# Optimization experiments

Hardware: AMD Instinct MI355X
Metric: run time of the kernel (lower is better)

## Reference

```python
import jax, jax.numpy as jnp
import numpy as np
import math

LN_EPS = 1e-5
EPS = 1e-8

def _unfold3(x, stride):
    # torch nn.Unfold(kernel_size=3, stride=stride, padding=1); output [B, C*9, L]
    B, C, H, W = x.shape
    xp = jnp.pad(x, ((0, 0), (0, 0), (1, 1), (1, 1)))
    Ho = (H + 2 - 3) // stride + 1
    Wo = (W + 2 - 3) // stride + 1
    pats = [xp[:, :, i:i + stride * (Ho - 1) + 1:stride, j:j + stride * (Wo - 1) + 1:stride]
            for i in range(3) for j in range(3)]
    out = jnp.stack(pats, axis=2)  # [B,C,9,Ho,Wo]  (c-major, then kh,kw: torch ordering)
    return out.reshape(B, C * 9, Ho * Wo)

def _ln(x, g, b):
    mu = jnp.mean(x, axis=-1, keepdims=True)
    var = jnp.mean((x - mu) ** 2, axis=-1, keepdims=True)
    return (x - mu) * jax.lax.rsqrt(var + LN_EPS) * g + b

def _prm_exp(x, w):
    # x: [B,T,emb], w: [m,emb] -> [B,T,m]
    m = w.shape[0]
    xd = jnp.sum(x * x, axis=-1, keepdims=True) / 2.0
    wtx = jnp.einsum('bte,me->btm', x, w)
    return jnp.exp(wtx - xd) / math.sqrt(m)

def _performer(x, kqv_w, kqv_b, pw, pb, g1, b1, g2, b2, m1w, m1b, m2w, m2b, w):
    # Token_performer.forward (dropout = identity, eval mode)
    h = _ln(x, g1, b1)
    kqv = h @ kqv_w.T + kqv_b
    k, q, v = jnp.split(kqv, 3, axis=-1)  # torch.split order: k, q, v
    kp = _prm_exp(k, w)
    qp = _prm_exp(q, w)
    D = jnp.einsum('btm,bm->bt', qp, kp.sum(axis=1))[..., None]        # [B,T,1]
    kptv = jnp.einsum('btn,btm->bnm', v, kp)                            # [B,emb,m]
    y = jnp.einsum('btm,bnm->btn', qp, kptv) / (D + EPS)                # [B,T,emb]
    y = v + (y @ pw.T + pb)
    h2 = _ln(y, g2, b2)
    mlp = jax.nn.gelu(h2 @ m1w.T + m1b, approximate=False) @ m2w.T + m2b
    return y + mlp

def _forward(x,
             p1_kqv_w, p1_kqv_b, p1_proj_w, p1_proj_b, p1_n1_g, p1_n1_b, p1_n2_g, p1_n2_b,
             p1_m1_w, p1_m1_b, p1_m2_w, p1_m2_b, p1_w,
             p2_kqv_w, p2_kqv_b, p2_proj_w, p2_proj_b, p2_n1_g, p2_n1_b, p2_n2_g, p2_n2_b,
             p2_m1_w, p2_m1_b, p2_m2_w, p2_m2_b, p2_w,
             proj_w, proj_b):
    t = _unfold3(x, 1).transpose(0, 2, 1)  # [B, 50176, 27]
    t = _performer(t, p1_kqv_w, p1_kqv_b, p1_proj_w, p1_proj_b, p1_n1_g, p1_n1_b,
                   p1_n2_g, p1_n2_b, p1_m1_w, p1_m1_b, p1_m2_w, p1_m2_b, p1_w)
    B, N, C = t.shape
    s = int(math.isqrt(N))
    t = t.transpose(0, 2, 1).reshape(B, C, s, s)
    t = _unfold3(t, 2).transpose(0, 2, 1)  # [B, 12544, 576]
    t = _performer(t, p2_kqv_w, p2_kqv_b, p2_proj_w, p2_proj_b, p2_n1_g, p2_n1_b,
                   p2_n2_g, p2_n2_b, p2_m1_w, p2_m1_b, p2_m2_w, p2_m2_b, p2_w)
    B, N, C = t.shape
    s = int(math.isqrt(N))
    t = t.transpose(0, 2, 1).reshape(B, C, s, s)
    t = _unfold3(t, 2).transpose(0, 2, 1)  # [B, 3136, 576]
    return t @ proj_w.T + proj_b           # [B, 3136, 768]

def setup_inputs() -> dict:
    key = jax.random.key(0)
    ks = iter(jax.random.split(key, 40))
    def rn(shape, scale=0.02):
        return (jax.random.normal(next(ks), shape, dtype=jnp.float32) * scale)
    EMB, M = 64, 32
    inp = {'x': jax.random.normal(next(ks), (8, 3, 224, 224), dtype=jnp.float32)}
    for pfx, dim in (('p1', 27), ('p2', 576)):
        inp[f'{pfx}_kqv_w'] = rn((3 * EMB, dim))
        inp[f'{pfx}_kqv_b'] = jnp.zeros((3 * EMB,), jnp.float32)
        inp[f'{pfx}_proj_w'] = rn((EMB, EMB))
        inp[f'{pfx}_proj_b'] = jnp.zeros((EMB,), jnp.float32)
        inp[f'{pfx}_n1_g'] = jnp.ones((dim,), jnp.float32)
        inp[f'{pfx}_n1_b'] = jnp.zeros((dim,), jnp.float32)
        inp[f'{pfx}_n2_g'] = jnp.ones((EMB,), jnp.float32)
        inp[f'{pfx}_n2_b'] = jnp.zeros((EMB,), jnp.float32)
        inp[f'{pfx}_m1_w'] = rn((EMB, EMB))
        inp[f'{pfx}_m1_b'] = jnp.zeros((EMB,), jnp.float32)
        inp[f'{pfx}_m2_w'] = rn((EMB, EMB))
        inp[f'{pfx}_m2_b'] = jnp.zeros((EMB,), jnp.float32)
        # frozen random-feature projection, scaled ~ orthogonal * sqrt(m)
        inp[f'{pfx}_w'] = jax.random.normal(next(ks), (M, EMB), dtype=jnp.float32)
    inp['proj_w'] = rn((768, 576))
    inp['proj_b'] = jnp.zeros((768,), jnp.float32)
    return inp

def reference(x,
              p1_kqv_w, p1_kqv_b, p1_proj_w, p1_proj_b, p1_n1_g, p1_n1_b, p1_n2_g, p1_n2_b,
              p1_m1_w, p1_m1_b, p1_m2_w, p1_m2_b, p1_w,
              p2_kqv_w, p2_kqv_b, p2_proj_w, p2_proj_b, p2_n1_g, p2_n1_b, p2_n2_g, p2_n2_b,
              p2_m1_w, p2_m1_b, p2_m2_w, p2_m2_b, p2_w,
              proj_w, proj_b):
    return _forward(x,
                    p1_kqv_w, p1_kqv_b, p1_proj_w, p1_proj_b, p1_n1_g, p1_n1_b, p1_n2_g, p1_n2_b,
                    p1_m1_w, p1_m1_b, p1_m2_w, p1_m2_b, p1_w,
                    p2_kqv_w, p2_kqv_b, p2_proj_w, p2_proj_b, p2_n1_g, p2_n1_b, p2_n2_g, p2_n2_b,
                    p2_m1_w, p2_m1_b, p2_m2_w, p2_m2_b, p2_w,
                    proj_w, proj_b)
```

## Files before the change

### kernel.cpp

```cpp
#include <hip/hip_runtime.h>
#include <hip/hip_bf16.h>
#include <math.h>

typedef __hip_bfloat16 bf16;
typedef __attribute__((ext_vector_type(8))) short frag8;
typedef __attribute__((ext_vector_type(4))) float f32x4;
typedef long long ll;

__device__ __forceinline__ float b2f(bf16 v) { return __bfloat162float(v); }
__device__ __forceinline__ bf16 f2b(float v) { return __float2bfloat16(v); }

__device__ __forceinline__ unsigned pk2f(float a, float b) {
    union { bf16 h[2]; unsigned u; } c;
    c.h[0] = f2b(a); c.h[1] = f2b(b);
    return c.u;
}
__device__ __forceinline__ void up8(const bf16* p, float* f) {
    const uint4 u = *(const uint4*)p;
    union { unsigned u; bf16 h[2]; } c;
    c.u = u.x; f[0] = b2f(c.h[0]); f[1] = b2f(c.h[1]);
    c.u = u.y; f[2] = b2f(c.h[0]); f[3] = b2f(c.h[1]);
    c.u = u.z; f[4] = b2f(c.h[0]); f[5] = b2f(c.h[1]);
    c.u = u.w; f[6] = b2f(c.h[0]); f[7] = b2f(c.h[1]);
}
__device__ __forceinline__ void up8u(const uint4 u, float* f) {
    union { unsigned u; bf16 h[2]; } c;
    c.u = u.x; f[0] = b2f(c.h[0]); f[1] = b2f(c.h[1]);
    c.u = u.y; f[2] = b2f(c.h[0]); f[3] = b2f(c.h[1]);
    c.u = u.z; f[4] = b2f(c.h[0]); f[5] = b2f(c.h[1]);
    c.u = u.w; f[6] = b2f(c.h[0]); f[7] = b2f(c.h[1]);
}

#define LN_EPS 1e-5f
#define D_EPS 1e-8f
#define INV_SQRT_M 0.17677669529663687f

__global__ __launch_bounds__(256) void k_sniff(const void* x, int* mode)
{
    __shared__ int cnt;
    if (threadIdx.x == 0) cnt = 0;
    __syncthreads();
    const unsigned short* u = (const unsigned short*)x;
    const unsigned short h = u[2 * threadIdx.x];
    const unsigned int bits = ((unsigned int)h) << 16;
    const float v = __uint_as_float(bits);
    const float a = fabsf(v);
    const bool sane = (h == 0) || (a >= 1e-8f && a <= 1e4f);
    if (!sane) atomicAdd(&cnt, 1);
    __syncthreads();
    if (threadIdx.x == 0) *mode = (cnt > 64) ? 1 : 0;
}

struct CvTab { const void* src[28]; int dstOff[28]; int cum[29]; };

__global__ __launch_bounds__(256) void k_convert_all(CvTab tab, bf16* base,
                                                     const int* mode)
{
    const int idx = blockIdx.x * 256 + threadIdx.x;
    if (idx >= tab.cum[28]) return;
    int s = 0;
    while (idx >= tab.cum[s + 1]) ++s;
    const int local = idx - tab.cum[s];
    const float v = (*mode) ? ((const float*)tab.src[s])[local]
                            : b2f(((const bf16*)tab.src[s])[local]);
    base[tab.dstOff[s] + local] = f2b(v);
}

__global__ __launch_bounds__(256) void k_prep(
    const void* __restrict__ w1raw, const int* __restrict__ mode,
    bf16* __restrict__ w1ph, bf16* __restrict__ w1pl)
{
    const int idx = blockIdx.x * 256 + threadIdx.x;
    if (idx >= 6144) return;
    const int o = idx >> 5, k = idx & 31;
    float v = 0.f;
    if (k < 27)
        v = (*mode) ? ((const float*)w1raw)[o * 27 + k]
                    : b2f(((const bf16*)w1raw)[o * 27 + k]);
    const bf16 h = f2b(v);
    w1ph[idx] = h;
    w1pl[idx] = f2b(v - b2f(h));
}

__global__ __launch_bounds__(256) void k_fused1(
    const bf16* __restrict__ x, const bf16* __restrict__ w1ph,
    const bf16* __restrict__ w1pl, const bf16* __restrict__ kqvb,
    const bf16* __restrict__ n1g, const bf16* __restrict__ n1b,
    const bf16* __restrict__ pw,
    bf16* __restrict__ KP, bf16* __restrict__ QP, bf16* __restrict__ V,
    float* __restrict__ red, const int b)
{
    __shared__ __align__(16) char smem[49632];
    bf16 (*wps)[72] = (bf16(*)[72])(smem);
    bf16 (*Ah)[40]  = (bf16(*)[40])(smem + 4608);
    bf16 (*Al)[40]  = (bf16(*)[40])(smem + 9728);
    bf16 (*Th)[72]  = (bf16(*)[72])(smem + 14848);
    bf16 (*Tl)[72]  = (bf16(*)[72])(smem + 24064);
    bf16 (*Wh)[40]  = (bf16(*)[40])(smem + 33280);
    bf16 (*Wl)[40]  = (bf16(*)[40])(smem + 38400);
    bf16 (*KPs)[40] = (bf16(*)[40])(smem + 43520);
    bf16 (*Vs)[72]  = (bf16(*)[72])(smem + 14848);
    float* kbs = (float*)(smem + 48640);
    float* gs  = (float*)(smem + 49408);
    float* bs  = (float*)(smem + 49520);

    const int tid = threadIdx.x;
    {
        const int i = tid * 8;
        *(uint4*)(&wps[i >> 6][i & 63]) = *(const uint4*)(pw + i);
    }
    if (tid < 192) kbs[tid] = b2f(kqvb[tid]);
    if (tid < 27) { gs[tid] = b2f(n1g[tid]); bs[tid] = b2f(n1b[tid]); }
    if (blockIdx.x == 0)
        for (int i = tid; i < 2080; i += 256) red[i] = 0.f;

    const int tok = tid >> 2, part = tid & 3;
    const int t = blockIdx.x * 64 + tok;
    const int h = t / 224, w = t - h * 224;
    const int d0 = part * 7;
    const int nd = (part == 3) ? 6 : 7;
    float vals[7];
    float s = 0.f;
    #pragma unroll
    for (int q = 0; q < 7; ++q) {
        float val = 0.f;
        if (q < nd) {
            const int d = d0 + q;
            const int c = d / 9, rr = d - c * 9;
            const int pi = rr / 3, pj = rr - pi * 3;
            const int hh = h + pi - 1, ww = w + pj - 1;
            if (hh >= 0 && hh < 224 && ww >= 0 && ww < 224)
                val = b2f(x[((ll)(b * 3 + c) * 224 + hh) * 224 + ww]);
        }
        vals[q] = val; s += val;
    }
    s += __shfl_xor(s, 1, 64);  s += __shfl_xor(s, 2, 64);
    const float mean = s * (1.f / 27.f);
    float s2 = 0.f;
    #pragma unroll
    for (int q = 0; q < 7; ++q) {
        if (q < nd) { const float dd = vals[q] - mean; s2 += dd * dd; }
    }
    s2 += __shfl_xor(s2, 1, 64); s2 += __shfl_xor(s2, 2, 64);
    const float rs = rsqrtf(s2 * (1.f / 27.f) + LN_EPS);
    __syncthreads();
    #pragma unroll
    for (int q = 0; q < 7; ++q) {
        if (q < nd) {
            const int d = d0 + q;
            const float nv = (vals[q] - mean) * rs * gs[d] + bs[d];
            const bf16 nh = f2b(nv);
            Ah[tok][d] = nh;
            Al[tok][d] = f2b(nv - b2f(nh));
        }
    }
    if (part == 3) {
        #pragma unroll
        for (int d = 27; d < 32; ++d) { Ah[tok][d] = f2b(0.f); Al[tok][d] = f2b(0.f); }
    }

    const int wv = tid >> 6, lane = tid & 63;
    const int l15 = lane & 15;
    const int k8 = (lane >> 4) << 3;
    const int rbase = (lane >> 4) << 2;
    const int srow = tid >> 2;
    const int scol = (tid & 3) << 3;
    const int colg = (tid & 3) << 4;

    float xdK[4], xdQ[4];

    #pragma unroll
    for (int g = 0; g < 3; ++g) {
        *(uint4*)(&Wh[srow][scol]) = *(const uint4*)(w1ph + (g * 64 + srow) * 32 + scol);
        *(uint4*)(&Wl[srow][scol]) = *(const uint4*)(w1pl + (g * 64 + srow) * 32 + scol);
        __syncthreads();
        const frag8 ah = *(const frag8*)(&Ah[(wv << 4) + l15][k8]);
        const frag8 al = *(const frag8*)(&Al[(wv << 4) + l15][k8]);
        f32x4 acc[4] = {};
        #pragma unroll
        for (int nt = 0; nt < 4; ++nt) {
            const frag8 bh = *(const frag8*)(&Wh[(nt << 4) + l15][k8]);
            const frag8 bl = *(const frag8*)(&Wl[(nt << 4) + l15][k8]);
            acc[nt] = __builtin_amdgcn_mfma_f32_16x16x32_bf16(ah, bh, acc[nt], 0, 0, 0);
            acc[nt] = __builtin_amdgcn_mfma_f32_16x16x32_bf16(al, bh, acc[nt], 0, 0, 0);
            acc[nt] = __builtin_amdgcn_mfma_f32_16x16x32_bf16(ah, bl, acc[nt], 0, 0, 0);
            acc[nt] = __builtin_amdgcn_mfma_f32_16x16x32_bf16(al, bl, acc[nt], 0, 0, 0);
        }
        float xdp[4] = {0.f, 0.f, 0.f, 0.f};
        #pragma unroll
        for (int nt = 0; nt < 4; ++nt) {
            const int col = (nt << 4) + l15;
            const float bv = kbs[g * 64 + col];
            #pragma unroll
            for (int r = 0; r < 4; ++r) {
                const float tb = acc[nt][r] + bv;
                const int trow = (wv << 4) + rbase + r;
                if (g < 2) {
                    const bf16 th = f2b(tb);
                    Th[trow][col] = th;
                    Tl[trow][col] = f2b(tb - b2f(th));
                    xdp[r] += tb * tb;
                } else {
                    Vs[trow][col] = f2b(tb);
                }
            }
        }
        if (g < 2) {
            #pragma unroll
            for (int r = 0; r < 4; ++r) {
                float v = xdp[r];
                v += __shfl_xor(v, 1, 64); v += __shfl_xor(v, 2, 64);
                v += __shfl_xor(v, 4, 64); v += __shfl_xor(v, 8, 64);
                if (g == 0) xdK[r] = 0.5f * v; else xdQ[r] = 0.5f * v;
            }
        }
        __syncthreads();
        if (g < 2) {
            f32x4 acc2[2] = {};
            #pragma unroll
            for (int k0 = 0; k0 < 64; k0 += 32) {
                const frag8 ath = *(const frag8*)(&Th[(wv << 4) + l15][k8 + k0]);
                const frag8 atl = *(const frag8*)(&Tl[(wv << 4) + l15][k8 + k0]);
                #pragma unroll
                for (int nt = 0; nt < 2; ++nt) {
                    const frag8 bw = *(const frag8*)(&wps[(nt << 4) + l15][k8 + k0]);
                    acc2[nt] = __builtin_amdgcn_mfma_f32_16x16x32_bf16(ath, bw, acc2[nt], 0, 0, 0);
                    acc2[nt] = __builtin_amdgcn_mfma_f32_16x16x32_bf16(atl, bw, acc2[nt], 0, 0, 0);
                }
            }
            #pragma unroll
            for (int nt = 0; nt < 2; ++nt)
                #pragma unroll
                for (int r = 0; r < 4; ++r) {
                    const float xd = (g == 0) ? xdK[r] : xdQ[r];
                    const float p = expf(fminf(acc2[nt][r] - xd, 30.f)) * INV_SQRT_M;
                    KPs[(wv << 4) + rbase + r][(nt << 4) + l15] = f2b(p);
                }
            __syncthreads();
            bf16* dstP = (g == 0 ? KP : QP) + ((ll)blockIdx.x * 64 + srow) * 32 + scol;
            *(uint4*)dstP = *(const uint4*)(&KPs[srow][scol]);
            __syncthreads();
        } else {
            bf16* dstV = V + ((ll)blockIdx.x * 64 + srow) * 64 + colg;
            *(uint4*)dstV       = *(const uint4*)(&Vs[srow][colg]);
            *(uint4*)(dstV + 8) = *(const uint4*)(&Vs[srow][colg + 8]);
        }
    }
}

__global__ __launch_bounds__(256) void k_reduce(
    const bf16* __restrict__ kpB, const bf16* __restrict__ vB, const int vstride,
    const int T, float* __restrict__ redBase, const int chunk)
{
    __shared__ bf16 VT[64][72];
    __shared__ bf16 KT[32][72];
    const int bz = blockIdx.y;
    const bf16* kp = kpB + (ll)bz * T * 32;
    const bf16* v  = vB + (ll)bz * T * (ll)vstride;
    float* red = redBase + (ll)bz * 2080;
    const int tid = threadIdx.x;
    const int wv = tid >> 6, lane = tid & 63;
    const int l15 = lane & 15, k8 = (lane >> 4) << 3, rbase = (lane >> 4) << 2;
    const int t0 = blockIdx.x * chunk;

    frag8 ones;
    {
        union { bf16 h; short s; } u; u.h = f2b(1.f);
        #pragma unroll
        for (int i = 0; i < 8; ++i) ones[i] = u.s;
    }

    f32x4 acc[2] = {};
    f32x4 accK[2] = {};

    for (int tt = 0; tt < chunk; tt += 64) {
        const int tb = t0 + tt;
        __syncthreads();
        {
            const int tk = tid >> 2, n0 = (tid & 3) << 4;
            const bf16* src = v + (ll)(tb + tk) * vstride + n0;
            bf16 tmp[16];
            *(uint4*)tmp       = *(const uint4*)src;
            *(uint4*)(tmp + 8) = *(const uint4*)(src + 8);
            #pragma unroll
            for (int j = 0; j < 16; ++j) VT[n0 + j][tk] = tmp[j];
        }
        {
            const int tk = tid >> 2, m0 = (tid & 3) << 3;
            const bf16* src = kp + (ll)(tb + tk) * 32 + m0;
            bf16 tmp[8];
            *(uint4*)tmp = *(const uint4*)src;
            #pragma unroll
            for (int j = 0; j < 8; ++j) KT[m0 + j][tk] = tmp[j];
        }
        __syncthreads();
        #pragma unroll
        for (int ks = 0; ks < 2; ++ks) {
            const frag8 af = *(const frag8*)(&VT[(wv << 4) + l15][k8 + ks * 32]);
            #pragma unroll
            for (int tn = 0; tn < 2; ++tn) {
                const frag8 bfv = *(const frag8*)(&KT[(tn << 4) + l15][k8 + ks * 32]);
                acc[tn] = __builtin_amdgcn_mfma_f32_16x16x32_bf16(af, bfv, acc[tn], 0, 0, 0);
            }
            if (wv == 0) {
                #pragma unroll
                for (int tn = 0; tn < 2; ++tn) {
                    const frag8 bfv = *(const frag8*)(&KT[(tn << 4) + l15][k8 + ks * 32]);
                    accK[tn] = __builtin_amdgcn_mfma_f32_16x16x32_bf16(ones, bfv, accK[tn], 0, 0, 0);
                }
            }
        }
    }
    #pragma unroll
    for (int tn = 0; tn < 2; ++tn) {
        const int m = (tn << 4) + l15;
        #pragma unroll
        for (int r = 0; r < 4; ++r) {
            const int n = (wv << 4) + rbase + r;
            atomicAdd(&red[n * 32 + m], acc[tn][r]);
        }
    }
    if (wv == 0 && (lane >> 4) == 0) {
        #pragma unroll
        for (int tn = 0; tn < 2; ++tn)
            atomicAdd(&red[2048 + (tn << 4) + l15], accK[tn][0]);
    }
}

__global__ __launch_bounds__(256) void k_postmlp(
    const bf16* __restrict__ qpB, const float* __restrict__ redBase,
    const bf16* __restrict__ vB, const int vstride,
    const bf16* __restrict__ pw, const bf16* __restrict__ pb,
    const bf16* __restrict__ n2g, const bf16* __restrict__ n2b,
    const bf16* __restrict__ w1, const bf16* __restrict__ b1,
    const bf16* __restrict__ w2, const bf16* __restrict__ b2,
    bf16* outB, const int T)
{
    __shared__ __align__(16) char smem[47232];
    bf16 (*QPs)[40] = (bf16(*)[40])(smem);
    bf16 (*KH)[40]  = (bf16(*)[40])(smem + 5120);
    bf16 (*KL)[40]  = (bf16(*)[40])(smem + 10240);
    float (*Cs)[72] = (float(*)[72])(smem);
    bf16 (*W1s)[72] = (bf16(*)[72])(smem);
    bf16 (*W2s)[72] = (bf16(*)[72])(smem + 9216);
    bf16 (*PWs)[72] = (bf16(*)[72])(smem + 18432);
    bf16 (*Gs)[72]  = (bf16(*)[72])(smem + 18432);
    bf16 (*Y0H)[72] = (bf16(*)[72])(smem + 27648);
    bf16 (*Ys)[72]  = (bf16(*)[72])(smem + 27648);
    bf16 (*Y0L)[72] = (bf16(*)[72])(smem + 36864);
    bf16 (*Hn)[72]  = (bf16(*)[72])(smem + 36864);
    float* invs  = (float*)(smem + 46080);
    float* pbs   = (float*)(smem + 46336);
    float* ksums = (float*)(smem + 46592);
    float* mns   = (float*)(smem + 46720);
    float* rss   = (float*)(smem + 46976);

    const int tid = threadIdx.x;
    const int bz = blockIdx.y;
    const float* red = redBase + (ll)bz * 2080;
    const bf16* qp = qpB + (ll)bz * (ll)T * 32;
    const bf16* v  = vB + (ll)bz * (ll)T * (ll)vstride;
    bf16* out = outB + (ll)bz * (ll)T * 64;
    const ll m0 = (ll)blockIdx.x * 64;

    const int lr = tid >> 2;
    const int lc8 = (tid & 3) << 3;
    const int lc16 = (tid & 3) << 4;

    *(uint4*)(&QPs[lr][lc8]) = *(const uint4*)(qp + (m0 + lr) * 32 + lc8);
    *(uint4*)(&PWs[lr][lc16])     = *(const uint4*)(pw + lr * 64 + lc16);
    *(uint4*)(&PWs[lr][lc16 + 8]) = *(const uint4*)(pw + lr * 64 + lc16 + 8);
    {
        const int i0 = tid * 8;
        const float4 a = *(const float4*)(red + i0);
        const float4 b = *(const float4*)(red + i0 + 4);
        const int n = i0 >> 5, m = i0 & 31;
        float xs[8] = {a.x, a.y, a.z, a.w, b.x, b.y, b.z, b.w};
        #pragma unroll
        for (int k = 0; k < 8; ++k) {
            const bf16 h = f2b(xs[k]);
            KH[n][m + k] = h;
            KL[n][m + k] = f2b(xs[k] - b2f(h));
        }
    }
    if (tid < 32) ksums[tid] = red[2048 + tid];
    if (tid < 64) pbs[tid] = b2f(pb[tid]);
    __syncthreads();

    if (tid < 64) {
        float D = D_EPS;
        #pragma unroll
        for (int m = 0; m < 32; ++m) D += b2f(QPs[tid][m]) * ksums[m];
        invs[tid] = 1.f / D;
    }

    const int wv = tid >> 6, lane = tid & 63;
    const int l15 = lane & 15;
    const int mr = (wv << 4) + l15;
    const int k8 = (lane >> 4) << 3;
    const int rbase = (lane >> 4) << 2;

    f32x4 acc[4] = {};
    {
        const frag8 af = *(const frag8*)(&QPs[mr][k8]);
        #pragma unroll
        for (int tn = 0; tn < 4; ++tn) {
            const int nr = (tn << 4) + l15;
            const frag8 bh = *(const frag8*)(&KH[nr][k8]);
            acc[tn] = __builtin_amdgcn_mfma_f32_16x16x32_bf16(af, bh, acc[tn], 0, 0, 0);
            const frag8 bl = *(const frag8*)(&KL[nr][k8]);
            acc[tn] = __builtin_amdgcn_mfma_f32_16x16x32_bf16(af, bl, acc[tn], 0, 0, 0);
        }
    }
    #pragma unroll
    for (int tn = 0; tn < 4; ++tn) {
        const int n = (tn << 4) + l15;
        #pragma unroll
        for (int r = 0; r < 4; ++r) {
            const float x = acc[tn][r];
            const bf16 h = f2b(x);
            Y0H[(wv << 4) + rbase + r][n] = h;
            Y0L[(wv << 4) + rbase + r][n] = f2b(x - b2f(h));
        }
    }
    __syncthreads();

    f32x4 acc2[4] = {};
    #pragma unroll
    for (int k0 = 0; k0 < 64; k0 += 32) {
        const frag8 ah = *(const frag8*)(&Y0H[mr][k8 + k0]);
        const frag8 al = *(const frag8*)(&Y0L[mr][k8 + k0]);
        #pragma unroll
        for (int tn = 0; tn < 4; ++tn) {
            const frag8 bw = *(const frag8*)(&PWs[(tn << 4) + l15][k8 + k0]);
            acc2[tn] = __builtin_amdgcn_mfma_f32_16x16x32_bf16(ah, bw, acc2[tn], 0, 0, 0);
            acc2[tn] = __builtin_amdgcn_mfma_f32_16x16x32_bf16(al, bw, acc2[tn], 0, 0, 0);
        }
    }
    #pragma unroll
    for (int tn = 0; tn < 4; ++tn) {
        const int n = (tn << 4) + l15;
        #pragma unroll
        for (int r = 0; r < 4; ++r) {
            const int row = (wv << 4) + rbase + r;
            Cs[row][n] = acc2[tn][r] * invs[row] + pbs[n];
        }
    }
    __syncthreads();

    {
        const int row = tid >> 2;
        const bf16* vsrc = v + (m0 + row) * (ll)vstride + lc16;
        #pragma unroll
        for (int hh = 0; hh < 2; ++hh) {
            float vv[8];
            up8(vsrc + hh * 8, vv);
            const float* cp = &Cs[row][lc16 + hh * 8];
            uint4 st;
            st.x = pk2f(cp[0] + vv[0], cp[1] + vv[1]);
            st.y = pk2f(cp[2] + vv[2], cp[3] + vv[3]);
            st.z = pk2f(cp[4] + vv[4], cp[5] + vv[5]);
            st.w = pk2f(cp[6] + vv[6], cp[7] + vv[7]);
            *(uint4*)(&Ys[row][lc16 + hh * 8]) = st;
        }
    }
    __syncthreads();

    if (tid < 64) {
        float s = 0.f, s2 = 0.f;
        #pragma unroll
        for (int n = 0; n < 64; ++n) { const float vv = b2f(Ys[tid][n]); s += vv; s2 += vv * vv; }
        const float mn = s * (1.f / 64.f);
        const float var = fmaxf(s2 * (1.f / 64.f) - mn * mn, 0.f);
        mns[tid] = mn; rss[tid] = rsqrtf(var + LN_EPS);
    }
    *(uint4*)(&W1s[lr][lc16])     = *(const uint4*)(w1 + lr * 64 + lc16);
    *(uint4*)(&W1s[lr][lc16 + 8]) = *(const uint4*)(w1 + lr * 64 + lc16 + 8);
    *(uint4*)(&W2s[lr][lc16])     = *(const uint4*)(w2 + lr * 64 + lc16);
    *(uint4*)(&W2s[lr][lc16 + 8]) = *(const uint4*)(w2 + lr * 64 + lc16 + 8);
    __syncthreads();

    for (int i = tid; i < 4096; i += 256) {
        const int r = i >> 6, c = i & 63;
        Hn[r][c] = f2b((b2f(Ys[r][c]) - mns[r]) * rss[r] * b2f(n2g[c]) + b2f(n2b[c]));
    }
    __syncthreads();

    f32x4 accm[4] = {};
    #pragma unroll
    for (int k0 = 0; k0 < 64; k0 += 32) {
        const frag8 af = *(const frag8*)(&Hn[mr][k8 + k0]);
        #pragma unroll
        for (int tn = 0; tn < 4; ++tn) {
            const frag8 bfv = *(const frag8*)(&W1s[(tn << 4) + l15][k8 + k0]);
            accm[tn] = __builtin_amdgcn_mfma_f32_16x16x32_bf16(af, bfv, accm[tn], 0, 0, 0);
        }
    }
    #pragma unroll
    for (int tn = 0; tn < 4; ++tn) {
        const int n = (tn << 4) + l15;
        const float bv = b2f(b1[n]);
        #pragma unroll
        for (int r = 0; r < 4; ++r) {
            float vg = accm[tn][r] + bv;
            vg = 0.5f * vg * (1.f + erff(vg * 0.70710678118654752f));
            Gs[(wv << 4) + rbase + r][n] = f2b(vg);
        }
    }
    __syncthreads();

    f32x4 accn[4] = {};
    #pragma unroll
    for (int k0 = 0; k0 < 64; k0 += 32) {
        const frag8 af = *(const frag8*)(&Gs[mr][k8 + k0]);
        #pragma unroll
        for (int tn = 0; tn < 4; ++tn) {
            const frag8 bfv = *(const frag8*)(&W2s[(tn << 4) + l15][k8 + k0]);
            accn[tn] = __builtin_amdgcn_mfma_f32_16x16x32_bf16(af, bfv, accn[tn], 0, 0, 0);
        }
    }
    #pragma unroll
    for (int tn = 0; tn < 4; ++tn) {
        const int n = (tn << 4) + l15;
        const float bv = b2f(b2[n]);
        #pragma unroll
        for (int r = 0; r < 4; ++r)
            Hn[(wv << 4) + rbase + r][n] = f2b(accn[tn][r] + bv);
    }
    __syncthreads();

    {
        const int row = tid >> 2;
        bf16* dst = out + (m0 + row) * 64 + lc16;
        #pragma unroll
        for (int hh = 0; hh < 2; ++hh) {
            float sv[8], rv[8];
            up8(&Hn[row][lc16 + hh * 8], sv);
            up8(&Ys[row][lc16 + hh * 8], rv);
            uint4 st;
            st.x = pk2f(sv[0] + rv[0], sv[1] + rv[1]);
            st.y = pk2f(sv[2] + rv[2], sv[3] + rv[3]);
            st.z = pk2f(sv[4] + rv[4], sv[5] + rv[5]);
            st.w = pk2f(sv[6] + rv[6], sv[7] + rv[7]);
            *(uint4*)(dst + hh * 8) = st;
        }
    }
}

__global__ __launch_bounds__(256) void k_unfold576(
    const bf16* __restrict__ in, const int Hin, const int Ho,
    const bf16* __restrict__ g, const bf16* __restrict__ bb,
    const int do_ln, bf16* __restrict__ A,
    const ll inBStride, const ll outBStride)
{
    in += (ll)blockIdx.y * inBStride;
    A  += (ll)blockIdx.y * outBStride;
    const int t = blockIdx.x * 4 + (threadIdx.x >> 6);
    const int l = threadIdx.x & 63;
    const int ho = t / Ho, wo = t - ho * Ho;
    float vals[9];
    float s = 0.f;
    #pragma unroll
    for (int r = 0; r < 9; ++r) {
        const int d = l + (r << 6);
        const int c = d / 9;
        const int rr = d - c * 9;
        const int i = rr / 3, j = rr - i * 3;
        const int hh = 2 * ho + i - 1, ww = 2 * wo + j - 1;
        float val = 0.f;
        if (hh >= 0 && hh < Hin && ww >= 0 && ww < Hin)
            val = b2f(in[((ll)hh * Hin + ww) * 64 + c]);
        vals[r] = val; s += val;
    }
    bf16* out = A + (ll)t * 576;
    if (do_ln) {
        #pragma unroll
        for (int o = 32; o > 0; o >>= 1) s += __shfl_xor(s, o, 64);
        const float mean = s * (1.f / 576.f);
        float s2 = 0.f;
        #pragma unroll
        for (int r = 0; r < 9; ++r) { const float dd = vals[r] - mean; s2 += dd * dd; }
        #pragma unroll
        for (int o = 32; o > 0; o >>= 1) s2 += __shfl_xor(s2, o, 64);
        const float rs = rsqrtf(s2 * (1.f / 576.f) + LN_EPS);
        #pragma unroll
        for (int r = 0; r < 9; ++r) {
            const int d = l + (r << 6);
            out[d] = f2b((vals[r] - mean) * rs * b2f(g[d]) + b2f(bb[d]));
        }
    } else {
        #pragma unroll
        for (int r = 0; r < 9; ++r) out[l + (r << 6)] = f2b(vals[r]);
    }
}

__global__ __launch_bounds__(256) void k_gemm(
    const bf16* __restrict__ A, const int lda,
    const bf16* __restrict__ W,
    const bf16* __restrict__ bias,
    const bf16* res, const int ldres,
    void* C, const int ldc, const ll mOff,
    const int K, const int* outm)
{
    __shared__ bf16 As[2][64][40];
    __shared__ bf16 Bs[2][64][40];
    __shared__ bf16 Cs[64][72];
    const int tid = threadIdx.x;
    const int wv = tid >> 6;
    const int lane = tid & 63;
    const ll m0 = (ll)blockIdx.x * 64;
    const int n0 = blockIdx.y * 64;
    f32x4 acc[4] = {};
    const int lr = tid >> 2;
    const int lc = (tid & 3) << 3;
    const int mr = (wv << 4) + (lane & 15);
    const int k8 = (lane >> 4) << 3;
    const bf16* Ag = A + (m0 + lr) * (ll)lda + lc;
    const bf16* Wg = W + (ll)(n0 + lr) * K + lc;

    uint4 av  = *(const uint4*)(Ag);
    uint4 wv4 = *(const uint4*)(Wg);
    *(uint4*)(&As[0][lr][lc]) = av;
    *(uint4*)(&Bs[0][lr][lc]) = wv4;
    int cur = 0;
    __syncthreads();
    for (int k0 = 0; k0 < K; k0 += 32) {
        const bool nxt = (k0 + 32 < K);
        if (nxt) {
            av  = *(const uint4*)(Ag + k0 + 32);
            wv4 = *(const uint4*)(Wg + k0 + 32);
        }
        const frag8 af = *(const frag8*)(&As[cur][mr][k8]);
        #pragma unroll
        for (int tn = 0; tn < 4; ++tn) {
            const frag8 bfv = *(const frag8*)(&Bs[cur][(tn << 4) + (lane & 15)][k8]);
            acc[tn] = __builtin_amdgcn_mfma_f32_16x16x32_bf16(af, bfv, acc[tn], 0, 0, 0);
        }
        if (nxt) {
            *(uint4*)(&As[cur ^ 1][lr][lc]) = av;
            *(uint4*)(&Bs[cur ^ 1][lr][lc]) = wv4;
        }
        __syncthreads();
        cur ^= 1;
    }
    const int om = outm ? *outm : 0;
    const int rbase = (lane >> 4) << 2;
    if (om) {
        #pragma unroll
        for (int tn = 0; tn < 4; ++tn) {
            const int n = n0 + (tn << 4) + (lane & 15);
            const float bv = bias ? b2f(bias[n]) : 0.f;
            #pragma unroll
            for (int r = 0; r < 4; ++r) {
                const ll m = m0 + (wv << 4) + rbase + r;
                float v = acc[tn][r] + bv;
                if (res) v += b2f(res[m * (ll)ldres + n]);
                ((float*)C)[(m + mOff) * (ll)ldc + n] = v;
            }
        }
        return;
    }
    #pragma unroll
    for (int tn = 0; tn < 4; ++tn) {
        const int nl = (tn << 4) + (lane & 15);
        const float bv = bias ? b2f(bias[n0 + nl]) : 0.f;
        #pragma unroll
        for (int r = 0; r < 4; ++r) {
            const ll m = m0 + (wv << 4) + rbase + r;
            float v = acc[tn][r] + bv;
            if (res) v += b2f(res[m * (ll)ldres + n0 + nl]);
            Cs[(wv << 4) + rbase + r][nl] = f2b(v);
        }
    }
    __syncthreads();
    const int row = tid >> 2;
    const int colg = (tid & 3) << 4;
    bf16* dst = (bf16*)C + (m0 + mOff + row) * (ll)ldc + n0 + colg;
    *(uint4*)dst       = *(const uint4*)(&Cs[row][colg]);
    *(uint4*)(dst + 8) = *(const uint4*)(&Cs[row][colg + 8]);
}

__global__ __launch_bounds__(256) void k_gemm128(
    const bf16* __restrict__ A, const int lda,
    const bf16* __restrict__ W,
    const bf16* __restrict__ bias,
    void* C, const int ldc, const ll mOff,
    const int K, const int* outm, const int gridN)
{
    __shared__ __align__(16) char smem[40960];
    bf16 (*As)[128][40] = (bf16(*)[128][40])smem;
    bf16 (*Bs)[128][40] = (bf16(*)[128][40])(smem + 20480);
    bf16 (*Cs)[136]     = (bf16(*)[136])smem;

    const int nwg = gridDim.x;
    const int orig = blockIdx.x;
    const int xcd = orig & 7;
    const int q = nwg >> 3, r = nwg & 7;
    const int wgid = (xcd < r ? xcd * (q + 1) : r * (q + 1) + (xcd - r) * q)
                     + (orig >> 3);
    const int mTile = wgid / gridN;
    const int nTile = wgid - mTile * gridN;
    const ll m0 = (ll)mTile * 128;
    const int n0 = nTile * 128;

    const int tid = threadIdx.x;
    const int wv = tid >> 6, lane = tid & 63, l15 = lane & 15;
    const int k8 = (lane >> 4) << 3;
    const int rbase = (lane >> 4) << 2;
    const int mr0 = (wv << 5) + l15;
    const int sr = tid >> 1, sc = (tid & 1) << 4;
    const bf16* Ag = A + (m0 + sr) * (ll)lda + sc;
    const bf16* Wg = W + (ll)(n0 + sr) * K + sc;

    f32x4 acc[2][8] = {};
    uint4 a0 = *(const uint4*)(Ag);
    uint4 a1 = *(const uint4*)(Ag + 8);
    uint4 b0 = *(const uint4*)(Wg);
    uint4 b1 = *(const uint4*)(Wg + 8);
    *(uint4*)(&(*As)[sr][sc])     = a0;
    *(uint4*)(&(*As)[sr][sc + 8]) = a1;
    *(uint4*)(&(*Bs)[sr][sc])     = b0;
    *(uint4*)(&(*Bs)[sr][sc + 8]) = b1;
    int cur = 0;
    __syncthreads();
    for (int k0 = 0; k0 < K; k0 += 32) {
        const bool nxt = (k0 + 32 < K);
        if (nxt) {
            a0 = *(const uint4*)(Ag + k0 + 32);
            a1 = *(const uint4*)(Ag + k0 + 40);
            b0 = *(const uint4*)(Wg + k0 + 32);
            b1 = *(const uint4*)(Wg + k0 + 40);
        }
        const frag8 af0 = *(const frag8*)(&As[cur][mr0][k8]);
        const frag8 af1 = *(const frag8*)(&As[cur][mr0 + 16][k8]);
        #pragma unroll
        for (int tn = 0; tn < 8; ++tn) {
            const frag8 bfv = *(const frag8*)(&Bs[cur][(tn << 4) + l15][k8]);
            acc[0][tn] = __builtin_amdgcn_mfma_f32_16x16x32_bf16(af0, bfv, acc[0][tn], 0, 0, 0);
            acc[1][tn] = __builtin_amdgcn_mfma_f32_16x16x32_bf16(af1, bfv, acc[1][tn], 0, 0, 0);
        }
        if (nxt) {
            *(uint4*)(&As[cur ^ 1][sr][sc])     = a0;
            *(uint4*)(&As[cur ^ 1][sr][sc + 8]) = a1;
            *(uint4*)(&Bs[cur ^ 1][sr][sc])     = b0;
            *(uint4*)(&Bs[cur ^ 1][sr][sc + 8]) = b1;
        }
        __syncthreads();
        cur ^= 1;
    }
    const int om = outm ? *outm : 0;
    if (om) {
        #pragma unroll
        for (int mi = 0; mi < 2; ++mi)
            #pragma unroll
            for (int tn = 0; tn < 8; ++tn) {
                const int n = n0 + (tn << 4) + l15;
                const float bv = bias ? b2f(bias[n]) : 0.f;
                #pragma unroll
                for (int rr2 = 0; rr2 < 4; ++rr2) {
                    const ll m = m0 + (wv << 5) + (mi << 4) + rbase + rr2;
                    ((float*)C)[(m + mOff) * (ll)ldc + n] = acc[mi][tn][rr2] + bv;
                }
            }
        return;
    }
    #pragma unroll
    for (int mi = 0; mi < 2; ++mi)
        #pragma unroll
        for (int tn = 0; tn < 8; ++tn) {
            const int nl = (tn << 4) + l15;
            const float bv = bias ? b2f(bias[n0 + nl]) : 0.f;
            #pragma unroll
            for (int rr2 = 0; rr2 < 4; ++rr2)
                Cs[(wv << 5) + (mi << 4) + rbase + rr2][nl] = f2b(acc[mi][tn][rr2] + bv);
        }
    __syncthreads();
    const int row = tid >> 1;
    const int colg = (tid & 1) << 6;
    bf16* dst = (bf16*)C + (m0 + mOff + row) * (ll)ldc + n0 + colg;
    #pragma unroll
    for (int u = 0; u < 8; ++u)
        *(uint4*)(dst + u * 8) = *(const uint4*)(&Cs[row][colg + u * 8]);
}

__global__ __launch_bounds__(256) void k_fusedP2(
    const bf16* __restrict__ kqv, const bf16* __restrict__ pw,
    bf16* __restrict__ KP, bf16* __restrict__ QP,
    float* __restrict__ redBase, const int T)
{
    __shared__ __align__(16) char smem[19200];
    bf16 (*Ks)[72]  = (bf16(*)[72])(smem);
    bf16 (*wps)[72] = (bf16(*)[72])(smem + 9216);
    bf16 (*KPs)[40] = (bf16(*)[40])(smem + 13824);
    float* xds = (float*)(smem + 18944);

    const int tid = threadIdx.x;
    const int bz = blockIdx.y;
    {
        const int i = tid * 8;
        *(uint4*)(&wps[i >> 6][i & 63]) = *(const uint4*)(pw + i);
    }
    if (blockIdx.x == 0) {
        float* red = redBase + (ll)bz * 2080;
        for (int i = tid; i < 2080; i += 256) red[i] = 0.f;
    }
    const ll gt0 = (ll)bz * T + (ll)blockIdx.x * 64;
    const int srow = tid >> 2;
    const int colg = (tid & 3) << 4;
    const int scol = (tid & 3) << 3;
    const int wv = tid >> 6, lane = tid & 63;
    const int l15 = lane & 15, k8 = (lane >> 4) << 3, rbase = (lane >> 4) << 2;

    #pragma unroll
    for (int p = 0; p < 2; ++p) {
        const bf16* src = kqv + (gt0 + srow) * 192 + p * 64 + colg;
        const uint4 u0 = *(const uint4*)src;
        const uint4 u1 = *(const uint4*)(src + 8);
        *(uint4*)(&Ks[srow][colg])     = u0;
        *(uint4*)(&Ks[srow][colg + 8]) = u1;
        float f0[8], f1[8];
        up8u(u0, f0); up8u(u1, f1);
        float s2 = 0.f;
        #pragma unroll
        for (int k = 0; k < 8; ++k) s2 += f0[k] * f0[k] + f1[k] * f1[k];
        s2 += __shfl_xor(s2, 1, 64); s2 += __shfl_xor(s2, 2, 64);
        if ((tid & 3) == 0) xds[srow] = 0.5f * s2;
        __syncthreads();
        f32x4 acc2[2] = {};
        #pragma unroll
        for (int k0 = 0; k0 < 64; k0 += 32) {
            const frag8 af = *(const frag8*)(&Ks[(wv << 4) + l15][k8 + k0]);
            #pragma unroll
            for (int nt = 0; nt < 2; ++nt) {
                const frag8 bw = *(const frag8*)(&wps[(nt << 4) + l15][k8 + k0]);
                acc2[nt] = __builtin_amdgcn_mfma_f32_16x16x32_bf16(af, bw, acc2[nt], 0, 0, 0);
            }
        }
        #pragma unroll
        for (int nt = 0; nt < 2; ++nt)
            #pragma unroll
            for (int r = 0; r < 4; ++r) {
                const int trow = (wv << 4) + rbase + r;
                const float pv = expf(fminf(acc2[nt][r] - xds[trow], 30.f)) * INV_SQRT_M;
                KPs[trow][(nt << 4) + l15] = f2b(pv);
            }
        __syncthreads();
        bf16* dst = (p == 0 ? KP : QP) + (gt0 + srow) * 32 + scol;
        *(uint4*)dst = *(const uint4*)(&KPs[srow][scol]);
        __syncthreads();
    }
}

extern "C" void kernel_launch(void* const* d_in, const int* in_sizes, int n_in,
                              void* d_out, int out_size, void* d_ws, size_t ws_size,
                              hipStream_t stream)
{
    (void)in_sizes; (void)n_in; (void)out_size;
    const int T1 = 50176, T2 = 12544;
    char* ws = (char*)d_ws;

    size_t cur = 0;
    auto alloc = [&](size_t bytes) {
        size_t r = cur; cur += (bytes + 127) & ~(size_t)127; return r;
    };
    static const int segIdx[28] = {0, 2, 3, 4, 5, 6, 7, 8, 9, 10, 11, 12, 13,
                                   14, 15, 16, 17, 18, 19, 20, 21, 22, 23, 24, 25, 26, 27, 28};
    static const int segN[28] = {1204224, 192, 4096, 64, 27, 27, 64, 64, 4096, 64, 4096, 64, 2048,
                                 110592, 192, 4096, 64, 576, 576, 64, 64, 4096, 64, 4096, 64, 2048,
                                 442368, 768};
    size_t segOff[28];
    for (int i = 0; i < 28; ++i) segOff[i] = alloc((size_t)segN[i] * 2);
    const size_t oMODE = alloc(256);
    const size_t oRED  = alloc(66560);
    const size_t oW1P  = alloc(24576);
    const size_t oBIG  = alloc(6422528);
    const size_t oKP   = alloc(3211264);
    const size_t oQP   = alloc(3211264);
    (void)oQP;

    bf16* P[28];
    for (int i = 0; i < 28; ++i) P[i] = (bf16*)(ws + segOff[i]);
    bf16* XC = P[0];
    bf16 *P1KQVB = P[1], *P1PW = P[2], *P1PB = P[3], *P1N1G = P[4], *P1N1B = P[5];
    bf16 *P1N2G = P[6], *P1N2B = P[7], *P1M1W = P[8], *P1M1B = P[9], *P1M2W = P[10];
    bf16 *P1M2B = P[11], *P1W = P[12];
    bf16 *P2KQVW = P[13], *P2KQVB = P[14], *P2PW = P[15], *P2PB = P[16];
    bf16 *P2N1G = P[17], *P2N1B = P[18], *P2N2G = P[19], *P2N2B = P[20];
    bf16 *P2M1W = P[21], *P2M1B = P[22], *P2M2W = P[23], *P2M2B = P[24], *P2W = P[25];
    bf16 *PROJW = P[26], *PROJB = P[27];

    int*   MODE = (int*)(ws + oMODE);
    float* REDF = (float*)(ws + oRED);
    bf16*  W1PH = (bf16*)(ws + oW1P);
    bf16*  W1PL = (bf16*)(ws + oW1P + 12288);
    bf16*  BIG  = (bf16*)(ws + oBIG);
    bf16*  KP   = (bf16*)(ws + oKP);
    bf16*  QP   = (bf16*)(ws + oKP + 3211264);
    bf16*  A2   = (bf16*)(ws + oKP);
    bf16*  KQV2F = (bf16*)d_out;
    bf16*  KP2F  = (bf16*)(ws + oKP);
    bf16*  QP2F  = (bf16*)(ws + oKP + 6422528);
    bf16*  YB2F  = (bf16*)(ws + oBIG);
    bf16*  A3c   = (bf16*)(ws + oBIG + 12845056);

    k_sniff<<<1, 256, 0, stream>>>(d_in[0], MODE);
    CvTab tab;
    int cum = 0;
    for (int i = 0; i < 28; ++i) {
        tab.src[i] = d_in[segIdx[i]];
        tab.dstOff[i] = (int)(segOff[i] / 2);
        tab.cum[i] = cum;
        cum += segN[i];
    }
    tab.cum[28] = cum;
    k_convert_all<<<(cum + 255) / 256, 256, 0, stream>>>(tab, (bf16*)ws, MODE);
    k_prep<<<24, 256, 0, stream>>>(d_in[1], MODE, W1PH, W1PL);

    for (int b = 0; b < 8; ++b) {
        float* REDb = REDF + (ll)b * 2080;
        k_fused1<<<784, 256, 0, stream>>>(XC, W1PH, W1PL, P1KQVB, P1N1G, P1N1B,
                                          P1W, KP, QP, BIG, REDb, b);
        k_reduce<<<dim3(392, 1), 256, 0, stream>>>(KP, BIG, 64, T1, REDb, 128);
        k_postmlp<<<dim3(784, 1), 256, 0, stream>>>(QP, REDb, BIG, 64, P1PW, P1PB,
            P1N2G, P1N2B, P1M1W, P1M1B, P1M2W, P1M2B, BIG, T1);
        k_unfold576<<<dim3(3136, 1), 256, 0, stream>>>(BIG, 224, 112, P2N1G, P2N1B,
                                                       1, A2, 0, 0);
        k_gemm<<<dim3(196, 3), 256, 0, stream>>>(A2, 576, P2KQVW, P2KQVB,
            nullptr, 0, KQV2F, 192, (ll)b * T2, 576, nullptr);
    }

    k_fusedP2<<<dim3(196, 8), 256, 0, stream>>>(KQV2F, P2W, KP2F, QP2F, REDF, T2);
    k_reduce<<<dim3(98, 8), 256, 0, stream>>>(KP2F, KQV2F + 128, 192, T2, REDF, 128);
    k_postmlp<<<dim3(196, 8), 256, 0, stream>>>(QP2F, REDF, KQV2F + 128, 192,
        P2PW, P2PB, P2N2G, P2N2B, P2M1W, P2M1B, P2M2W, P2M2B, YB2F, T2);

    const size_t needFull = oBIG + 12845056 + (size_t)25088 * 576 * 2;
    if (ws_size >= needFull) {
        bf16* A3 = (bf16*)(ws + oBIG + 12845056);
        k_unfold576<<<dim3(784, 8), 256, 0, stream>>>(
            YB2F, 112, 56, nullptr, nullptr, 0, A3, (ll)T2 * 64, (ll)3136 * 576);
        k_gemm128<<<1176, 256, 0, stream>>>(A3, 576, PROJW, PROJB,
            d_out, 768, 0, 576, MODE, 6);
    } else {
        for (int c = 0; c < 4; ++c) {
            k_unfold576<<<dim3(784, 2), 256, 0, stream>>>(
                YB2F + (ll)(2 * c) * T2 * 64, 112, 56, nullptr, nullptr, 0,
                A3c, (ll)T2 * 64, (ll)3136 * 576);
            k_gemm128<<<294, 256, 0, stream>>>(A3c, 576, PROJW, PROJB,
                d_out, 768, (ll)c * 6272, 576, MODE, 6);
        }
    }
}
```

Measured before the change: 963.6 us.

## Fuse stage-1 kptv/ksum reduction into k_fused1 with per-block atomics

The stage-1 reduction (V^T·KP and the KP column sum) now runs inside k_fused1 on each 64-token tile, using shared-memory transposes and MFMA, with results accumulated into the global buffer by atomics. This drops the separate k_reduce launch per batch and the write and re-read of KP through global memory. Zeroing of the reduction buffer moves to k_prep for all batches at once. In exchange there are many float atomics per block and an extra shared-memory transpose phase.

```diff
diff --git a/kernel.cpp b/kernel.cpp
--- a/kernel.cpp
+++ b/kernel.cpp
@@ -68,9 +68,10 @@
 
 __global__ __launch_bounds__(256) void k_prep(
     const void* __restrict__ w1raw, const int* __restrict__ mode,
-    bf16* __restrict__ w1ph, bf16* __restrict__ w1pl)
+    bf16* __restrict__ w1ph, bf16* __restrict__ w1pl, float* __restrict__ redf)
 {
     const int idx = blockIdx.x * 256 + threadIdx.x;
+    if (idx < 16640) redf[idx] = 0.f;
     if (idx >= 6144) return;
     const int o = idx >> 5, k = idx & 31;
     float v = 0.f;
@@ -87,7 +88,7 @@
     const bf16* __restrict__ w1pl, const bf16* __restrict__ kqvb,
     const bf16* __restrict__ n1g, const bf16* __restrict__ n1b,
     const bf16* __restrict__ pw,
-    bf16* __restrict__ KP, bf16* __restrict__ QP, bf16* __restrict__ V,
+    bf16* __restrict__ QP, bf16* __restrict__ V,
     float* __restrict__ red, const int b)
 {
     __shared__ __align__(16) char smem[49632];
@@ -100,6 +101,9 @@
     bf16 (*Wl)[40]  = (bf16(*)[40])(smem + 38400);
     bf16 (*KPs)[40] = (bf16(*)[40])(smem + 43520);
     bf16 (*Vs)[72]  = (bf16(*)[72])(smem + 14848);
+    bf16 (*Qst)[40] = (bf16(*)[40])(smem + 33280);
+    bf16 (*KT)[72]  = (bf16(*)[72])(smem);
+    bf16 (*VT)[72]  = (bf16(*)[72])(smem + 4608);
     float* kbs = (float*)(smem + 48640);
     float* gs  = (float*)(smem + 49408);
     float* bs  = (float*)(smem + 49520);
@@ -111,8 +115,6 @@
     }
     if (tid < 192) kbs[tid] = b2f(kqvb[tid]);
     if (tid < 27) { gs[tid] = b2f(n1g[tid]); bs[tid] = b2f(n1b[tid]); }
-    if (blockIdx.x == 0)
-        for (int i = tid; i < 2080; i += 256) red[i] = 0.f;
 
     const int tok = tid >> 2, part = tid & 3;
     const int t = blockIdx.x * 64 + tok;
@@ -228,23 +230,86 @@
                     acc2[nt] = __builtin_amdgcn_mfma_f32_16x16x32_bf16(atl, bw, acc2[nt], 0, 0, 0);
                 }
             }
-            #pragma unroll
-            for (int nt = 0; nt < 2; ++nt)
+            if (g == 0) {
                 #pragma unroll
-                for (int r = 0; r < 4; ++r) {
-                    const float xd = (g == 0) ? xdK[r] : xdQ[r];
-                    const float p = expf(fminf(acc2[nt][r] - xd, 30.f)) * INV_SQRT_M;
-                    KPs[(wv << 4) + rbase + r][(nt << 4) + l15] = f2b(p);
-                }
-            __syncthreads();
-            bf16* dstP = (g == 0 ? KP : QP) + ((ll)blockIdx.x * 64 + srow) * 32 + scol;
-            *(uint4*)dstP = *(const uint4*)(&KPs[srow][scol]);
-            __syncthreads();
+                for (int nt = 0; nt < 2; ++nt)
+                    #pragma unroll
+                    for (int r = 0; r < 4; ++r) {
+                        const float p = expf(fminf(acc2[nt][r] - xdK[r], 30.f)) * INV_SQRT_M;
+                        KPs[(wv << 4) + rbase + r][(nt << 4) + l15] = f2b(p);
+                    }
+            } else {
+                #pragma unroll
+                for (int nt = 0; nt < 2; ++nt)
+                    #pragma unroll
+                    for (int r = 0; r < 4; ++r) {
+                        const float p = expf(fminf(acc2[nt][r] - xdQ[r], 30.f)) * INV_SQRT_M;
+                        Qst[(wv << 4) + rbase + r][(nt << 4) + l15] = f2b(p);
+                    }
+                __syncthreads();
+                bf16* dstP = QP + ((ll)blockIdx.x * 64 + srow) * 32 + scol;
+                *(uint4*)dstP = *(const uint4*)(&Qst[srow][scol]);
+                __syncthreads();
+            }
         } else {
             bf16* dstV = V + ((ll)blockIdx.x * 64 + srow) * 64 + colg;
             *(uint4*)dstV       = *(const uint4*)(&Vs[srow][colg]);
             *(uint4*)(dstV + 8) = *(const uint4*)(&Vs[srow][colg + 8]);
         }
+    }
+
+    {
+        const int tk = tid >> 2, n0v = (tid & 3) << 4;
+        bf16 tmp[16];
+        *(uint4*)tmp       = *(const uint4*)(&Vs[tk][n0v]);
+        *(uint4*)(tmp + 8) = *(const uint4*)(&Vs[tk][n0v + 8]);
+        #pragma unroll
+        for (int j = 0; j < 16; ++j) VT[n0v + j][tk] = tmp[j];
+        const int m0k = (tid & 3) << 3;
+        bf16 tmp2[8];
+        *(uint4*)tmp2 = *(const uint4*)(&KPs[tk][m0k]);
+        #pragma unroll
+        for (int j = 0; j < 8; ++j) KT[m0k + j][tk] = tmp2[j];
+    }
+    __syncthreads();
+
+    frag8 ones;
+    {
+        union { bf16 hh2; short ss; } u; u.hh2 = f2b(1.f);
+        #pragma unroll
+        for (int i = 0; i < 8; ++i) ones[i] = u.ss;
+    }
+    f32x4 racc[2] = {};
+    f32x4 raccK[2] = {};
+    #pragma unroll
+    for (int ks = 0; ks < 2; ++ks) {
+        const frag8 af = *(const frag8*)(&VT[(wv << 4) + l15][k8 + ks * 32]);
+        #pragma unroll
+        for (int tn = 0; tn < 2; ++tn) {
+            const frag8 bfv = *(const frag8*)(&KT[(tn << 4) + l15][k8 + ks * 32]);
+            racc[tn] = __builtin_amdgcn_mfma_f32_16x16x32_bf16(af, bfv, racc[tn], 0, 0, 0);
+        }
+        if (wv == 0) {
+            #pragma unroll
+            for (int tn = 0; tn < 2; ++tn) {
+                const frag8 bfv = *(const frag8*)(&KT[(tn << 4) + l15][k8 + ks * 32]);
+                raccK[tn] = __builtin_amdgcn_mfma_f32_16x16x32_bf16(ones, bfv, raccK[tn], 0, 0, 0);
+            }
+        }
+    }
+    #pragma unroll
+    for (int tn = 0; tn < 2; ++tn) {
+        const int m = (tn << 4) + l15;
+        #pragma unroll
+        for (int r = 0; r < 4; ++r) {
+            const int n = (wv << 4) + rbase + r;
+            atomicAdd(&red[n * 32 + m], racc[tn][r]);
+        }
+    }
+    if (wv == 0 && (lane >> 4) == 0) {
+        #pragma unroll
+        for (int tn = 0; tn < 2; ++tn)
+            atomicAdd(&red[2048 + (tn << 4) + l15], raccK[tn][0]);
     }
 }
 
@@ -894,7 +959,6 @@
     bf16*  W1PH = (bf16*)(ws + oW1P);
     bf16*  W1PL = (bf16*)(ws + oW1P + 12288);
     bf16*  BIG  = (bf16*)(ws + oBIG);
-    bf16*  KP   = (bf16*)(ws + oKP);
     bf16*  QP   = (bf16*)(ws + oKP + 3211264);
     bf16*  A2   = (bf16*)(ws + oKP);
     bf16*  KQV2F = (bf16*)d_out;
@@ -914,13 +978,12 @@
     }
     tab.cum[28] = cum;
     k_convert_all<<<(cum + 255) / 256, 256, 0, stream>>>(tab, (bf16*)ws, MODE);
-    k_prep<<<24, 256, 0, stream>>>(d_in[1], MODE, W1PH, W1PL);
+    k_prep<<<65, 256, 0, stream>>>(d_in[1], MODE, W1PH, W1PL, REDF);
 
     for (int b = 0; b < 8; ++b) {
         float* REDb = REDF + (ll)b * 2080;
         k_fused1<<<784, 256, 0, stream>>>(XC, W1PH, W1PL, P1KQVB, P1N1G, P1N1B,
-                                          P1W, KP, QP, BIG, REDb, b);
-        k_reduce<<<dim3(392, 1), 256, 0, stream>>>(KP, BIG, 64, T1, REDb, 128);
+                                          P1W, QP, BIG, REDb, b);
         k_postmlp<<<dim3(784, 1), 256, 0, stream>>>(QP, REDb, BIG, 64, P1PW, P1PB,
             P1N2G, P1N2B, P1M1W, P1M1B, P1M2W, P1M2B, BIG, T1);
         k_unfold576<<<dim3(3136, 1), 256, 0, stream>>>(BIG, 224, 112, P2N1G, P2N1B,
```

After: 966.3 us. No clear change (+0.3%).
